# Kernel tuning notes

Measured on AMD Instinct MI355X. Metric: run time of the kernel, lower is better.

Reference implementation:

```python
import jax, jax.numpy as jnp
import numpy as np


def setup_inputs() -> dict:
    key = jax.random.key(0)
    k1, k2, k3 = jax.random.split(key, 3)
    B, S, H, L = 64, 512, 768, 9  # batch, seq_len, bert hidden, num_labels
    sequence_output = jax.random.normal(k1, (B, S, H), dtype=jnp.float32)
    valid_mask = jax.random.randint(k2, (B, S), 0, 2, dtype=jnp.int32)
    W = jax.random.normal(k3, (H, L), dtype=jnp.float32) * 0.02  # TruncatedNormal stddev ~ initializer_range
    b = jnp.zeros((L,), dtype=jnp.float32)
    return {"sequence_output": sequence_output, "valid_mask": valid_mask, "W": W, "b": b}


def reference(sequence_output, valid_mask, W, b):
    # Per-row stream compaction: tokens with valid_mask==1 are moved to the
    # front of their row (stable order); remaining slots stay zero.
    B, S, H = sequence_output.shape
    pos = jnp.cumsum(valid_mask, axis=1) - 1           # destination index for valid tokens
    safe = jnp.where(valid_mask == 1, pos, S)           # invalid tokens -> dump slot S
    batch = jnp.arange(B)[:, None]                      # [B,1]
    valid_output = (
        jnp.zeros((B, S + 1, H), dtype=sequence_output.dtype)
        .at[batch, safe]
        .set(sequence_output)
    )[:, :S]                                            # drop dump slot
    # dropout is identity at inference (training=False)
    logits = jax.nn.softmax(valid_output @ W + b, axis=-1)  # [B,S,L]
    return logits
```

## Files before the change

### kernel.cpp

```cpp
#include <hip/hip_runtime.h>

#define B_ 64
#define S_ 512
#define H_ 768
#define L_ 9
#define TPB 16
#define BPR (S_ / TPB)

__global__ __launch_bounds__(256) void ner_kernel(const float* __restrict__ seq,
                                                  const int* __restrict__ mask,
                                                  const float* __restrict__ W,
                                                  const float* __restrict__ bias,
                                                  float* __restrict__ out) {
    __shared__ float wt[L_ * 3 * 64 * 4];
    __shared__ float bsh[L_];
    __shared__ int   srcrow[S_];
    __shared__ int   wsum[4];

    const int tid  = threadIdx.x;
    const int lane = tid & 63;
    const int w    = tid >> 6;
    const int row  = blockIdx.x / BPR;
    const int sub  = blockIdx.x % BPR;

    for (int idx = tid; idx < L_ * 3 * 64 * 4; idx += 256) {
        int j    = idx & 3;
        int ln   = (idx >> 2) & 63;
        int rest = idx >> 8;
        int j4   = rest % 3;
        int cls  = rest / 3;
        wt[idx] = W[(12 * ln + 4 * j4 + j) * L_ + cls];
    }
    if (tid < L_) bsh[tid] = bias[tid];

    const int e0 = 2 * tid, e1 = 2 * tid + 1;
    const int v0 = (mask[row * S_ + e0] != 0);
    const int v1 = (mask[row * S_ + e1] != 0);
    const unsigned long long b0 = __ballot(v0);
    const unsigned long long b1 = __ballot(v1);
    const unsigned long long lt = (1ULL << lane) - 1ULL;
    const int pfx  = __popcll(b0 & lt) + __popcll(b1 & lt);
    const int wtot = __popcll(b0) + __popcll(b1);
    if (lane == 0) wsum[w] = wtot;
    __syncthreads();

    int woff = 0;
#pragma unroll
    for (int i = 0; i < 4; i++)
        if (i < w) woff += wsum[i];
    const int cnt = wsum[0] + wsum[1] + wsum[2] + wsum[3];
    const int p0  = woff + pfx;
    if (v0) srcrow[p0] = e0;
    if (v1) srcrow[p0 + v0] = e1;
    __syncthreads();

    const int basep = sub * TPB + w * 4;
    float x[4][12];
#pragma unroll
    for (int t = 0; t < 4; t++) {
        const int pp = basep + t;
        if (pp < cnt) {
            const int src = srcrow[pp];
            const float4* p4 = reinterpret_cast<const float4*>(
                seq + ((size_t)row * S_ + src) * H_ + lane * 12);
            float4 a0 = p4[0], a1 = p4[1], a2 = p4[2];
            x[t][0] = a0.x; x[t][1] = a0.y; x[t][2]  = a0.z; x[t][3]  = a0.w;
            x[t][4] = a1.x; x[t][5] = a1.y; x[t][6]  = a1.z; x[t][7]  = a1.w;
            x[t][8] = a2.x; x[t][9] = a2.y; x[t][10] = a2.z; x[t][11] = a2.w;
        } else {
#pragma unroll
            for (int k = 0; k < 12; k++) x[t][k] = 0.0f;
        }
    }

    float acc[4][L_];
#pragma unroll
    for (int t = 0; t < 4; t++)
#pragma unroll
        for (int c = 0; c < L_; c++) acc[t][c] = 0.0f;

    const float4* wt4 = reinterpret_cast<const float4*>(wt);
#pragma unroll
    for (int cls = 0; cls < L_; cls++) {
#pragma unroll
        for (int j4 = 0; j4 < 3; j4++) {
            float4 wv = wt4[(cls * 3 + j4) * 64 + lane];
#pragma unroll
            for (int t = 0; t < 4; t++) {
                acc[t][cls] += x[t][j4 * 4 + 0] * wv.x + x[t][j4 * 4 + 1] * wv.y
                             + x[t][j4 * 4 + 2] * wv.z + x[t][j4 * 4 + 3] * wv.w;
            }
        }
    }

#pragma unroll
    for (int t = 0; t < 4; t++) {
#pragma unroll
        for (int c = 0; c < L_; c++) {
            float v = acc[t][c];
            v += __shfl_xor(v, 1);
            v += __shfl_xor(v, 2);
            v += __shfl_xor(v, 4);
            v += __shfl_xor(v, 8);
            v += __shfl_xor(v, 16);
            v += __shfl_xor(v, 32);
            acc[t][c] = v;
        }
    }

    if (lane < 36) {
#pragma unroll
        for (int t = 0; t < 4; t++) {
            if (lane >= t * 9 && lane < t * 9 + 9) {
                const int c = lane - t * 9;
                float lg[L_];
                float m = -3.4e38f;
#pragma unroll
                for (int c2 = 0; c2 < L_; c2++) {
                    lg[c2] = acc[t][c2] + bsh[c2];
                    m = fmaxf(m, lg[c2]);
                }
                float s = 0.0f, mine = 0.0f;
#pragma unroll
                for (int c2 = 0; c2 < L_; c2++) {
                    float e = __expf(lg[c2] - m);
                    s += e;
                    if (c2 == c) mine = e;
                }
                out[((size_t)row * S_ + basep) * L_ + lane] = mine / s;
            }
        }
    }
}

extern "C" void kernel_launch(void* const* d_in, const int* in_sizes, int n_in,
                              void* d_out, int out_size, void* d_ws, size_t ws_size,
                              hipStream_t stream) {
    const float* seq  = (const float*)d_in[0];
    const int*   mask = (const int*)d_in[1];
    const float* W    = (const float*)d_in[2];
    const float* bias = (const float*)d_in[3];
    float*       out  = (float*)d_out;

    ner_kernel<<<B_ * BPR, 256, 0, stream>>>(seq, mask, W, bias, out);
}
```

Before: 161.6 us.

## Use butterfly transpose-reduction, two passes per block, coalesced weight staging

Replaces the per-class full-wave shuffle reductions with a recursive-halving butterfly: each lane ends up owning one class's partial sum, cutting shuffle count, and the softmax then runs across 16-lane groups in parallel. Each block now handles 32 tokens over two passes, halving the grid and so the number of times W is restaged and the mask is scanned. The W staging loop now reads global memory contiguously and scatters into shared memory. The cost is more loop structure and select logic per shuffle stage.

```diff
diff --git a/kernel.cpp b/kernel.cpp
--- a/kernel.cpp
+++ b/kernel.cpp
@@ -4,8 +4,9 @@
 #define S_ 512
 #define H_ 768
 #define L_ 9
-#define TPB 16
+#define TPB 32
 #define BPR (S_ / TPB)
+#define NPASS 2
 
 __global__ __launch_bounds__(256) void ner_kernel(const float* __restrict__ seq,
                                                   const int* __restrict__ mask,
@@ -13,7 +14,7 @@
                                                   const float* __restrict__ bias,
                                                   float* __restrict__ out) {
     __shared__ float wt[L_ * 3 * 64 * 4];
-    __shared__ float bsh[L_];
+    __shared__ float bsh[16];
     __shared__ int   srcrow[S_];
     __shared__ int   wsum[4];
 
@@ -23,15 +24,15 @@
     const int row  = blockIdx.x / BPR;
     const int sub  = blockIdx.x % BPR;
 
-    for (int idx = tid; idx < L_ * 3 * 64 * 4; idx += 256) {
-        int j    = idx & 3;
-        int ln   = (idx >> 2) & 63;
-        int rest = idx >> 8;
-        int j4   = rest % 3;
-        int cls  = rest / 3;
-        wt[idx] = W[(12 * ln + 4 * j4 + j) * L_ + cls];
+    for (int idx = tid; idx < H_ * L_; idx += 256) {
+        float val = W[idx];
+        int h  = idx / 9;
+        int c  = idx - 9 * h;
+        int ln = h / 12;
+        int r  = h - 12 * ln;
+        wt[((c * 3 + (r >> 2)) * 64 + ln) * 4 + (r & 3)] = val;
     }
-    if (tid < L_) bsh[tid] = bias[tid];
+    if (tid < 16) bsh[tid] = (tid < L_) ? bias[tid] : 0.0f;
 
     const int e0 = 2 * tid, e1 = 2 * tid + 1;
     const int v0 = (mask[row * S_ + e0] != 0);
@@ -54,82 +55,117 @@
     if (v1) srcrow[p0 + v0] = e1;
     __syncthreads();
 
-    const int basep = sub * TPB + w * 4;
-    float x[4][12];
-#pragma unroll
-    for (int t = 0; t < 4; t++) {
-        const int pp = basep + t;
-        if (pp < cnt) {
-            const int src = srcrow[pp];
-            const float4* p4 = reinterpret_cast<const float4*>(
-                seq + ((size_t)row * S_ + src) * H_ + lane * 12);
-            float4 a0 = p4[0], a1 = p4[1], a2 = p4[2];
-            x[t][0] = a0.x; x[t][1] = a0.y; x[t][2]  = a0.z; x[t][3]  = a0.w;
-            x[t][4] = a1.x; x[t][5] = a1.y; x[t][6]  = a1.z; x[t][7]  = a1.w;
-            x[t][8] = a2.x; x[t][9] = a2.y; x[t][10] = a2.z; x[t][11] = a2.w;
-        } else {
-#pragma unroll
-            for (int k = 0; k < 12; k++) x[t][k] = 0.0f;
-        }
-    }
-
-    float acc[4][L_];
-#pragma unroll
-    for (int t = 0; t < 4; t++)
-#pragma unroll
-        for (int c = 0; c < L_; c++) acc[t][c] = 0.0f;
+    const int cls = ((lane & 1) << 3) | (((lane >> 1) & 1) << 2)
+                  | (((lane >> 2) & 1) << 1) | ((lane >> 3) & 1);
+    const float bb = bsh[cls];
+    const int g = lane >> 4;
 
     const float4* wt4 = reinterpret_cast<const float4*>(wt);
+
+    for (int pass = 0; pass < NPASS; pass++) {
+        const int basep = sub * TPB + w * (4 * NPASS) + pass * 4;
+
+        float x[4][12];
 #pragma unroll
-    for (int cls = 0; cls < L_; cls++) {
+        for (int t = 0; t < 4; t++) {
+            const int pp = basep + t;
+            if (pp < cnt) {
+                const int src = srcrow[pp];
+                const float4* p4 = reinterpret_cast<const float4*>(
+                    seq + ((size_t)row * S_ + src) * H_ + lane * 12);
+                float4 a0 = p4[0], a1 = p4[1], a2 = p4[2];
+                x[t][0] = a0.x; x[t][1] = a0.y; x[t][2]  = a0.z; x[t][3]  = a0.w;
+                x[t][4] = a1.x; x[t][5] = a1.y; x[t][6]  = a1.z; x[t][7]  = a1.w;
+                x[t][8] = a2.x; x[t][9] = a2.y; x[t][10] = a2.z; x[t][11] = a2.w;
+            } else {
 #pragma unroll
-        for (int j4 = 0; j4 < 3; j4++) {
-            float4 wv = wt4[(cls * 3 + j4) * 64 + lane];
-#pragma unroll
-            for (int t = 0; t < 4; t++) {
-                acc[t][cls] += x[t][j4 * 4 + 0] * wv.x + x[t][j4 * 4 + 1] * wv.y
-                             + x[t][j4 * 4 + 2] * wv.z + x[t][j4 * 4 + 3] * wv.w;
+                for (int k = 0; k < 12; k++) x[t][k] = 0.0f;
             }
         }
-    }
+
+        float acc[4][L_];
+#pragma unroll
+        for (int t = 0; t < 4; t++)
+#pragma unroll
+            for (int c = 0; c < L_; c++) acc[t][c] = 0.0f;
 
 #pragma unroll
-    for (int t = 0; t < 4; t++) {
+        for (int c = 0; c < L_; c++) {
 #pragma unroll
-        for (int c = 0; c < L_; c++) {
-            float v = acc[t][c];
-            v += __shfl_xor(v, 1);
-            v += __shfl_xor(v, 2);
-            v += __shfl_xor(v, 4);
-            v += __shfl_xor(v, 8);
-            v += __shfl_xor(v, 16);
-            v += __shfl_xor(v, 32);
-            acc[t][c] = v;
+            for (int j4 = 0; j4 < 3; j4++) {
+                float4 wv = wt4[(c * 3 + j4) * 64 + lane];
+#pragma unroll
+                for (int t = 0; t < 4; t++) {
+                    acc[t][c] += x[t][j4 * 4 + 0] * wv.x + x[t][j4 * 4 + 1] * wv.y
+                               + x[t][j4 * 4 + 2] * wv.z + x[t][j4 * 4 + 3] * wv.w;
+                }
+            }
         }
-    }
 
-    if (lane < 36) {
+        float logit[4];
 #pragma unroll
         for (int t = 0; t < 4; t++) {
-            if (lane >= t * 9 && lane < t * 9 + 9) {
-                const int c = lane - t * 9;
-                float lg[L_];
-                float m = -3.4e38f;
+            float v[16];
 #pragma unroll
-                for (int c2 = 0; c2 < L_; c2++) {
-                    lg[c2] = acc[t][c2] + bsh[c2];
-                    m = fmaxf(m, lg[c2]);
+            for (int c = 0; c < L_; c++) v[c] = acc[t][c];
+#pragma unroll
+            for (int c = L_; c < 16; c++) v[c] = 0.0f;
+
+            {
+                const bool b = (lane & 1);
+#pragma unroll
+                for (int i = 0; i < 8; i++) {
+                    float give = b ? v[i] : v[i + 8];
+                    float got  = __shfl_xor(give, 1);
+                    v[i] = (b ? v[i + 8] : v[i]) + got;
                 }
-                float s = 0.0f, mine = 0.0f;
+            }
+            {
+                const bool b = ((lane >> 1) & 1);
 #pragma unroll
-                for (int c2 = 0; c2 < L_; c2++) {
-                    float e = __expf(lg[c2] - m);
-                    s += e;
-                    if (c2 == c) mine = e;
+                for (int i = 0; i < 4; i++) {
+                    float give = b ? v[i] : v[i + 4];
+                    float got  = __shfl_xor(give, 2);
+                    v[i] = (b ? v[i + 4] : v[i]) + got;
                 }
-                out[((size_t)row * S_ + basep) * L_ + lane] = mine / s;
             }
+            {
+                const bool b = ((lane >> 2) & 1);
+#pragma unroll
+                for (int i = 0; i < 2; i++) {
+                    float give = b ? v[i] : v[i + 2];
+                    float got  = __shfl_xor(give, 4);
+                    v[i] = (b ? v[i + 2] : v[i]) + got;
+                }
+            }
+            {
+                const bool b = ((lane >> 3) & 1);
+                float give = b ? v[0] : v[1];
+                float got  = __shfl_xor(give, 8);
+                v[0] = (b ? v[1] : v[0]) + got;
+            }
+            v[0] += __shfl_xor(v[0], 16);
+            v[0] += __shfl_xor(v[0], 32);
+            logit[t] = v[0];
         }
+
+        float lg = (g == 0) ? logit[0] : (g == 1) ? logit[1]
+                 : (g == 2) ? logit[2] : logit[3];
+        lg += bb;
+        float lx = (cls < L_) ? lg : -1e30f;
+        float m = lx;
+        m = fmaxf(m, __shfl_xor(m, 1));
+        m = fmaxf(m, __shfl_xor(m, 2));
+        m = fmaxf(m, __shfl_xor(m, 4));
+        m = fmaxf(m, __shfl_xor(m, 8));
+        float e = (cls < L_) ? __expf(lx - m) : 0.0f;
+        float ssum = e;
+        ssum += __shfl_xor(ssum, 1);
+        ssum += __shfl_xor(ssum, 2);
+        ssum += __shfl_xor(ssum, 4);
+        ssum += __shfl_xor(ssum, 8);
+        if (cls < L_)
+            out[((size_t)row * S_ + basep + g) * L_ + cls] = e / ssum;
     }
 }
 
```

Result: faster. 154.8 us (-4.2%).
